# Optimization experiments

Measured on AMD Instinct MI355X. Metric: run time of the kernel, lower is better.

The kernel has to match this reference:

```python
import jax, jax.numpy as jnp
import numpy as np

CACHE_SIZE = 500_000
TEACHER_DIM = 512
STUDENT_DIM = 128
N_TASKS = 8
BATCH = 16384


def setup_inputs() -> dict:
    key = jax.random.key(0)
    k1, k2, k3, k4, k5 = jax.random.split(key, 5)
    return {
        # GPU-resident KV-cache of precomputed teacher outputs (dict -> dense table)
        "cache_emb": jax.random.normal(k1, (CACHE_SIZE, TEACHER_DIM), dtype=jnp.float32),
        "cache_logits": jax.random.normal(k2, (CACHE_SIZE, N_TASKS), dtype=jnp.float32),
        # nn.Linear(teacher_dim, student_dim, bias=False) weight (stored as in-dim x out-dim)
        "W": (jax.random.normal(k3, (TEACHER_DIM, STUDENT_DIM), dtype=jnp.float32)
              / np.float32(np.sqrt(TEACHER_DIM))),
        # per-query cache slot (result of hashing (user_id, item_id) keys)
        "slot_idx": jax.random.randint(k4, (BATCH,), 0, CACHE_SIZE, dtype=jnp.int32),
        # True = cache hit, False = miss (TTL-expired / unseen) -> zero placeholder
        "hit_mask": jax.random.randint(k5, (BATCH,), 0, 2, dtype=jnp.int32).astype(bool),
    }


def reference(cache_emb, cache_logits, W, slot_idx, hit_mask):
    # query(): gather teacher embeddings/logits per key, zeros on miss, then project.
    hit = hit_mask[:, None]
    emb = jnp.where(hit, cache_emb[slot_idx], 0.0)          # (B, teacher_dim)
    teacher_feats = emb @ W                                  # (B, student_dim)
    teacher_logits = jnp.where(hit, cache_logits[slot_idx], 0.0)  # (B, n_tasks)
    return teacher_feats, teacher_logits
```

## Files before the change

kernel.cpp:

```cpp
#include <hip/hip_runtime.h>
#include <hip/hip_bf16.h>

#define TD 512
#define SD 128
#define NT 8
#define BATCH 16384
#define BR 64

typedef float f32x4 __attribute__((ext_vector_type(4)));
typedef short s16x8 __attribute__((ext_vector_type(8)));
typedef unsigned short u16;
typedef unsigned long long u64;

__device__ __forceinline__ u16 f2bf(float f) {
    return __builtin_bit_cast(u16, __float2bfloat16(f));
}
__device__ __forceinline__ u64 pack4bf(f32x4 v) {
    u16 a[4];
    #pragma unroll
    for (int j = 0; j < 4; ++j) a[j] = f2bf(v[j]);
    return __builtin_bit_cast(u64, *(ushort4*)a);
}

__global__ __launch_bounds__(512, 2) void fused_kernel(
    const float* __restrict__ emb,
    const float* __restrict__ clogits,
    const float* __restrict__ W,
    const int* __restrict__ slot,
    const int* __restrict__ hit,
    float* __restrict__ feats_out,
    float* __restrict__ logits_out)
{
    __shared__ __align__(16) char Al[BR * TD * 2];
    __shared__ __align__(16) char Wf[2][32768];

    const int tid  = threadIdx.x;
    const int w    = tid >> 6;
    const int lane = tid & 63;
    const int m0b  = blockIdx.x * BR;

    f32x4 rg[8][2];
    #pragma unroll
    for (int r = 0; r < 8; ++r) {
        const int grow = m0b + w * 8 + r;
        if (hit[grow]) {
            const float* rp = emb + (long)slot[grow] * TD + lane * 4;
            rg[r][0] = *(const f32x4*)rp;
            rg[r][1] = *(const f32x4*)(rp + 256);
        } else {
            rg[r][0] = (f32x4){0.f, 0.f, 0.f, 0.f};
            rg[r][1] = (f32x4){0.f, 0.f, 0.f, 0.f};
        }
    }

#define STAGE_LOAD(c, WS)                                                     \
    {                                                                         \
        _Pragma("unroll")                                                     \
        for (int i = 0; i < 4; ++i) {                                         \
            const int s = tid + 512 * i;                                      \
            const int kbase = (c) * 128 + ((s >> 6) & 3) * 32 +               \
                              ((s >> 4) & 3) * 8;                             \
            const int n = ((s >> 8) & 7) * 16 + (s & 15);                     \
            _Pragma("unroll")                                                 \
            for (int j = 0; j < 8; ++j)                                       \
                WS[i * 8 + j] = W[(kbase + j) * SD + n];                      \
        }                                                                     \
    }

#define STAGE_WRITE(buf, WS)                                                  \
    {                                                                         \
        _Pragma("unroll")                                                     \
        for (int i = 0; i < 4; ++i) {                                         \
            u16 v[8];                                                         \
            _Pragma("unroll")                                                 \
            for (int j = 0; j < 8; ++j) v[j] = f2bf(WS[i * 8 + j]);           \
            *(s16x8*)(Wf[buf] + (tid + 512 * i) * 16) = *(const s16x8*)v;     \
        }                                                                     \
    }

    const int lrow = m0b + (tid >> 3);
    const int lj   = tid & 7;
    float lv = 0.f;
    if (hit[lrow]) lv = clogits[(long)slot[lrow] * NT + lj];

    float wsA[32], wsB[32];
    STAGE_LOAD(0, wsA);

    #pragma unroll
    for (int r = 0; r < 8; ++r) {
        const int rowL = w * 8 + r;
        const int swz = (rowL & 7) << 4;
        const int b0 = (rowL << 10) | (lane << 3);
        *(u64*)(Al + (b0 ^ swz))         = pack4bf(rg[r][0]);
        *(u64*)(Al + ((b0 + 512) ^ swz)) = pack4bf(rg[r][1]);
    }
    logits_out[(long)lrow * NT + lj] = lv;

    STAGE_WRITE(0, wsA);
    STAGE_LOAD(1, wsB);

    const int g = w >> 1;
    const int h = w & 1;
    const int lr16 = lane & 15;
    const int kb   = lane >> 4;
    const int rowL = g * 16 + lr16;
    const int aswz = (rowL & 7) << 4;

    f32x4 acc[4];
    #pragma unroll
    for (int t = 0; t < 4; ++t) acc[t] = (f32x4){0.f, 0.f, 0.f, 0.f};

#define COMPUTE(c, buf)                                                       \
    {                                                                         \
        _Pragma("unroll")                                                     \
        for (int s4 = 0; s4 < 4; ++s4) {                                      \
            const int abyte = ((rowL << 10) |                                 \
                               ((c) * 256 + s4 * 64 + kb * 16)) ^ aswz;       \
            const s16x8 a = *(const s16x8*)(Al + abyte);                      \
            _Pragma("unroll")                                                 \
            for (int t = 0; t < 4; ++t) {                                     \
                const s16x8 b = *(const s16x8*)(Wf[buf] +                     \
                    (((h * 4 + t) * 4 + s4) * 64 + lane) * 16);               \
                acc[t] = __builtin_amdgcn_mfma_f32_16x16x32_bf16(             \
                             a, b, acc[t], 0, 0, 0);                          \
            }                                                                 \
        }                                                                     \
    }

    __syncthreads();
    COMPUTE(0, 0);
    STAGE_WRITE(1, wsB);
    STAGE_LOAD(2, wsA);
    __syncthreads();
    COMPUTE(1, 1);
    STAGE_WRITE(0, wsA);
    STAGE_LOAD(3, wsB);
    __syncthreads();
    COMPUTE(2, 0);
    STAGE_WRITE(1, wsB);
    __syncthreads();
    COMPUTE(3, 1);

#undef STAGE_LOAD
#undef STAGE_WRITE
#undef COMPUTE

    #pragma unroll
    for (int t = 0; t < 4; ++t)
        #pragma unroll
        for (int i = 0; i < 4; ++i)
            feats_out[(long)(m0b + g * 16 + kb * 4 + i) * SD +
                      (h * 4 + t) * 16 + lr16] = acc[t][i];
}

extern "C" void kernel_launch(void* const* d_in, const int* in_sizes, int n_in,
                              void* d_out, int out_size, void* d_ws, size_t ws_size,
                              hipStream_t stream) {
    const float* cache_emb    = (const float*)d_in[0];
    const float* cache_logits = (const float*)d_in[1];
    const float* W            = (const float*)d_in[2];
    const int*   slot_idx     = (const int*)d_in[3];
    const int*   hitm         = (const int*)d_in[4];

    float* feats_out  = (float*)d_out;
    float* logits_out = (float*)d_out + (long)BATCH * SD;

    fused_kernel<<<BATCH / BR, 512, 0, stream>>>(cache_emb, cache_logits, W,
                                                 slot_idx, hitm,
                                                 feats_out, logits_out);
}
```

Before: 14.98 us.

## Halve block to 32 rows and 256 threads with 8-stage W pipeline

Shrinks each block from 64 rows/512 threads to 32 rows/256 threads, doubling the grid to 512 blocks and halving LDS use per block. The W staging is split into eight 64-K chunks with a re-derived fragment layout and a double-buffered loop. The aim is more blocks per CU and better overlap of gather latency. In exchange, each block converts and stages the full W separately, so total W reads and bf16 conversions double, and there are more barriers.

```diff
diff --git a/kernel.cpp b/kernel.cpp
--- a/kernel.cpp
+++ b/kernel.cpp
@@ -5,7 +5,7 @@
 #define SD 128
 #define NT 8
 #define BATCH 16384
-#define BR 64
+#define BR 32
 
 typedef float f32x4 __attribute__((ext_vector_type(4)));
 typedef short s16x8 __attribute__((ext_vector_type(8)));
@@ -22,7 +22,7 @@
     return __builtin_bit_cast(u64, *(ushort4*)a);
 }
 
-__global__ __launch_bounds__(512, 2) void fused_kernel(
+__global__ __launch_bounds__(256, 2) void fused_kernel(
     const float* __restrict__ emb,
     const float* __restrict__ clogits,
     const float* __restrict__ W,
@@ -32,7 +32,7 @@
     float* __restrict__ logits_out)
 {
     __shared__ __align__(16) char Al[BR * TD * 2];
-    __shared__ __align__(16) char Wf[2][32768];
+    __shared__ __align__(16) char Wf[2][16384];
 
     const int tid  = threadIdx.x;
     const int w    = tid >> 6;
@@ -53,14 +53,20 @@
         }
     }
 
+    const int lrow = m0b + (tid >> 3);
+    const int lj   = tid & 7;
+    float lv = 0.f;
+    if (hit[lrow]) lv = clogits[(long)slot[lrow] * NT + lj];
+
 #define STAGE_LOAD(c, WS)                                                     \
     {                                                                         \
         _Pragma("unroll")                                                     \
         for (int i = 0; i < 4; ++i) {                                         \
-            const int s = tid + 512 * i;                                      \
-            const int kbase = (c) * 128 + ((s >> 6) & 3) * 32 +               \
-                              ((s >> 4) & 3) * 8;                             \
-            const int n = ((s >> 8) & 7) * 16 + (s & 15);                     \
+            const int s = tid + 256 * i;                                      \
+            const int lu = s & 63;                                            \
+            const int kbase = (c) * 64 + ((s >> 6) & 1) * 32 +                \
+                              ((lu >> 4)) * 8;                                \
+            const int n = (s >> 7) * 16 + (lu & 15);                          \
             _Pragma("unroll")                                                 \
             for (int j = 0; j < 8; ++j)                                       \
                 WS[i * 8 + j] = W[(kbase + j) * SD + n];                      \
@@ -71,17 +77,15 @@
     {                                                                         \
         _Pragma("unroll")                                                     \
         for (int i = 0; i < 4; ++i) {                                         \
+            const int s = tid + 256 * i;                                      \
+            const int lu = s & 63;                                            \
+            const int u = (((s >> 7) * 2 + ((s >> 6) & 1)) * 64 + lu);        \
             u16 v[8];                                                         \
             _Pragma("unroll")                                                 \
             for (int j = 0; j < 8; ++j) v[j] = f2bf(WS[i * 8 + j]);           \
-            *(s16x8*)(Wf[buf] + (tid + 512 * i) * 16) = *(const s16x8*)v;     \
+            *(s16x8*)(Wf[buf] + u * 16) = *(const s16x8*)v;                   \
         }                                                                     \
     }
-
-    const int lrow = m0b + (tid >> 3);
-    const int lj   = tid & 7;
-    float lv = 0.f;
-    if (hit[lrow]) lv = clogits[(long)slot[lrow] * NT + lj];
 
     float wsA[32], wsB[32];
     STAGE_LOAD(0, wsA);
@@ -113,14 +117,14 @@
 #define COMPUTE(c, buf)                                                       \
     {                                                                         \
         _Pragma("unroll")                                                     \
-        for (int s4 = 0; s4 < 4; ++s4) {                                      \
+        for (int s4 = 0; s4 < 2; ++s4) {                                      \
             const int abyte = ((rowL << 10) |                                 \
-                               ((c) * 256 + s4 * 64 + kb * 16)) ^ aswz;       \
+                               ((c) * 128 + s4 * 64 + kb * 16)) ^ aswz;       \
             const s16x8 a = *(const s16x8*)(Al + abyte);                      \
             _Pragma("unroll")                                                 \
             for (int t = 0; t < 4; ++t) {                                     \
                 const s16x8 b = *(const s16x8*)(Wf[buf] +                     \
-                    (((h * 4 + t) * 4 + s4) * 64 + lane) * 16);               \
+                    ((((h * 4 + t) * 2 + s4) * 64 + lane) * 16));             \
                 acc[t] = __builtin_amdgcn_mfma_f32_16x16x32_bf16(             \
                              a, b, acc[t], 0, 0, 0);                          \
             }                                                                 \
@@ -128,18 +132,19 @@
     }
 
     __syncthreads();
-    COMPUTE(0, 0);
-    STAGE_WRITE(1, wsB);
-    STAGE_LOAD(2, wsA);
-    __syncthreads();
-    COMPUTE(1, 1);
-    STAGE_WRITE(0, wsA);
-    STAGE_LOAD(3, wsB);
-    __syncthreads();
-    COMPUTE(2, 0);
-    STAGE_WRITE(1, wsB);
-    __syncthreads();
-    COMPUTE(3, 1);
+    #pragma unroll
+    for (int c = 0; c < 8; ++c) {
+        if (c & 1) COMPUTE(c, 1) else COMPUTE(c, 0);
+        if (c < 7) {
+            if (c & 1) { STAGE_WRITE((c + 1) & 1, wsA); }
+            else       { STAGE_WRITE((c + 1) & 1, wsB); }
+            if (c < 6) {
+                if (c & 1) { STAGE_LOAD(c + 2, wsB); }
+                else       { STAGE_LOAD(c + 2, wsA); }
+            }
+            __syncthreads();
+        }
+    }
 
 #undef STAGE_LOAD
 #undef STAGE_WRITE
@@ -165,7 +170,7 @@
     float* feats_out  = (float*)d_out;
     float* logits_out = (float*)d_out + (long)BATCH * SD;
 
-    fused_kernel<<<BATCH / BR, 512, 0, stream>>>(cache_emb, cache_logits, W,
+    fused_kernel<<<BATCH / BR, 256, 0, stream>>>(cache_emb, cache_logits, W,
                                                  slot_idx, hitm,
                                                  feats_out, logits_out);
 }
```

New measurement: 17.13 us. +14.3%, slower.

## Pre-convert W to bf16 fragments in prep kernel and stream via global_load_lds

Applied to the files above, without the earlier changes.

Adds a small prep kernel that converts W into bf16 MFMA fragment layout in workspace and also writes the logits gather. The main kernel then loads W tiles straight into LDS with global_load_lds instead of every block re-reading fp32 W, converting it and writing it to LDS through registers. This removes redundant per-block conversion work and register pressure. The cost is a second kernel launch and a dependency between the two kernels. Correctness relies on the async LDS loads being complete before the barriers, with no explicit vmcnt wait added.

```diff
diff --git a/kernel.cpp b/kernel.cpp
--- a/kernel.cpp
+++ b/kernel.cpp
@@ -21,15 +21,44 @@
     for (int j = 0; j < 4; ++j) a[j] = f2bf(v[j]);
     return __builtin_bit_cast(u64, *(ushort4*)a);
 }
+__device__ __forceinline__ void glds16(const void* g, void* l) {
+    __builtin_amdgcn_global_load_lds(
+        (const __attribute__((address_space(1))) unsigned int*)g,
+        (__attribute__((address_space(3))) unsigned int*)l, 16, 0, 0);
+}
+
+__global__ __launch_bounds__(256) void prep_kernel(
+    const float* __restrict__ W, const float* __restrict__ clogits,
+    const int* __restrict__ slot, const int* __restrict__ hit,
+    u16* __restrict__ WF, float* __restrict__ logits_out)
+{
+    const int gid = blockIdx.x * 256 + threadIdx.x;
+    {
+        const int row = gid >> 1;
+        const int j4 = (gid & 1) * 4;
+        f32x4 v = (f32x4){0.f, 0.f, 0.f, 0.f};
+        if (hit[row]) v = *(const f32x4*)(clogits + (long)slot[row] * NT + j4);
+        *(f32x4*)(logits_out + (long)row * NT + j4) = v;
+    }
+    if (gid < 8192) {
+        const int lane = gid & 63;
+        const int kidx = (gid >> 6) & 15;
+        const int cg   = gid >> 10;
+        const int n    = cg * 16 + (lane & 15);
+        const int k0   = kidx * 32 + (lane >> 4) * 8;
+        u16 v[8];
+        #pragma unroll
+        for (int j = 0; j < 8; ++j) v[j] = f2bf(W[(k0 + j) * SD + n]);
+        *(s16x8*)(WF + (long)gid * 8) = *(const s16x8*)v;
+    }
+}
 
 __global__ __launch_bounds__(512, 2) void fused_kernel(
     const float* __restrict__ emb,
-    const float* __restrict__ clogits,
-    const float* __restrict__ W,
+    const u16* __restrict__ WF,
     const int* __restrict__ slot,
     const int* __restrict__ hit,
-    float* __restrict__ feats_out,
-    float* __restrict__ logits_out)
+    float* __restrict__ feats_out)
 {
     __shared__ __align__(16) char Al[BR * TD * 2];
     __shared__ __align__(16) char Wf[2][32768];
@@ -53,38 +82,16 @@
         }
     }
 
-#define STAGE_LOAD(c, WS)                                                     \
+#define GLDS(c, buf)                                                          \
     {                                                                         \
         _Pragma("unroll")                                                     \
-        for (int i = 0; i < 4; ++i) {                                         \
-            const int s = tid + 512 * i;                                      \
-            const int kbase = (c) * 128 + ((s >> 6) & 3) * 32 +               \
-                              ((s >> 4) & 3) * 8;                             \
-            const int n = ((s >> 8) & 7) * 16 + (s & 15);                     \
-            _Pragma("unroll")                                                 \
-            for (int j = 0; j < 8; ++j)                                       \
-                WS[i * 8 + j] = W[(kbase + j) * SD + n];                      \
-        }                                                                     \
+        for (int s4 = 0; s4 < 4; ++s4)                                        \
+            glds16(WF + ((long)(w * 16 + (c) * 4 + s4) * 64 + lane) * 8,      \
+                   Wf[buf] + (w * 4 + s4) * 1024);                            \
     }
 
-#define STAGE_WRITE(buf, WS)                                                  \
-    {                                                                         \
-        _Pragma("unroll")                                                     \
-        for (int i = 0; i < 4; ++i) {                                         \
-            u16 v[8];                                                         \
-            _Pragma("unroll")                                                 \
-            for (int j = 0; j < 8; ++j) v[j] = f2bf(WS[i * 8 + j]);           \
-            *(s16x8*)(Wf[buf] + (tid + 512 * i) * 16) = *(const s16x8*)v;     \
-        }                                                                     \
-    }
-
-    const int lrow = m0b + (tid >> 3);
-    const int lj   = tid & 7;
-    float lv = 0.f;
-    if (hit[lrow]) lv = clogits[(long)slot[lrow] * NT + lj];
-
-    float wsA[32], wsB[32];
-    STAGE_LOAD(0, wsA);
+    GLDS(0, 0);
+    GLDS(1, 1);
 
     #pragma unroll
     for (int r = 0; r < 8; ++r) {
@@ -94,10 +101,6 @@
         *(u64*)(Al + (b0 ^ swz))         = pack4bf(rg[r][0]);
         *(u64*)(Al + ((b0 + 512) ^ swz)) = pack4bf(rg[r][1]);
     }
-    logits_out[(long)lrow * NT + lj] = lv;
-
-    STAGE_WRITE(0, wsA);
-    STAGE_LOAD(1, wsB);
 
     const int g = w >> 1;
     const int h = w & 1;
@@ -129,20 +132,16 @@
 
     __syncthreads();
     COMPUTE(0, 0);
-    STAGE_WRITE(1, wsB);
-    STAGE_LOAD(2, wsA);
     __syncthreads();
+    GLDS(2, 0);
     COMPUTE(1, 1);
-    STAGE_WRITE(0, wsA);
-    STAGE_LOAD(3, wsB);
     __syncthreads();
+    GLDS(3, 1);
     COMPUTE(2, 0);
-    STAGE_WRITE(1, wsB);
     __syncthreads();
     COMPUTE(3, 1);
 
-#undef STAGE_LOAD
-#undef STAGE_WRITE
+#undef GLDS
 #undef COMPUTE
 
     #pragma unroll
@@ -165,7 +164,10 @@
     float* feats_out  = (float*)d_out;
     float* logits_out = (float*)d_out + (long)BATCH * SD;
 
-    fused_kernel<<<BATCH / BR, 512, 0, stream>>>(cache_emb, cache_logits, W,
-                                                 slot_idx, hitm,
-                                                 feats_out, logits_out);
+    u16* WF = (u16*)d_ws;
+
+    prep_kernel<<<128, 256, 0, stream>>>(W, cache_logits, slot_idx, hitm,
+                                         WF, logits_out);
+    fused_kernel<<<BATCH / BR, 512, 0, stream>>>(cache_emb, WF,
+                                                 slot_idx, hitm, feats_out);
 }
```

Measured after the change: 17.84 us. 19.1% more time.
